# Performance work log

Measured on AMD Instinct MI355X. Metric: run time of the kernel, lower is better.

The kernel has to match this reference:

```python
import jax, jax.numpy as jnp
import numpy as np

NUM_HEADS = 16
HEAD_DIM = 64
MEMORY_SIZE = 65536
K_SIMILAR = 8
K_CONTIGUOUS = 2
SURPRISE_THRESHOLD = 0.5
EPS = 1e-8  # torch F.cosine_similarity eps


def setup_inputs() -> dict:
    key = jax.random.key(0)
    ks = jax.random.split(key, 6)
    B, H, S, HD = 4, NUM_HEADS, 8192, HEAD_DIM
    D = H * HD
    inputs = jax.random.normal(ks[0], (B, S, D), dtype=jnp.float32)
    q = jax.random.normal(ks[1], (B, H, S, HD), dtype=jnp.float32)
    k = jax.random.normal(ks[2], (B, H, S, HD), dtype=jnp.float32)
    v = jax.random.normal(ks[3], (B, H, S, HD), dtype=jnp.float32)
    attention_mask = jnp.ones((B, S), dtype=jnp.float32)
    events = jax.random.normal(ks[4], (MEMORY_SIZE, D), dtype=jnp.float32)
    return {"inputs": inputs, "q": q, "k": k, "v": v,
            "attention_mask": attention_mask, "events": events,
            "seq_len_q": 8192}


def _segment_mean(kf, seg, S):
    # kf: [S, D], seg: [S] int32 segment ids (exclusive cumsum of boundary mask)
    sums = jax.ops.segment_sum(kf, seg, num_segments=S)          # [S, D]
    cnts = jax.ops.segment_sum(jnp.ones_like(seg, jnp.float32), seg, num_segments=S)
    means = sums / jnp.maximum(cnts, 1.0)[:, None]
    return means, cnts


def reference(inputs, q, k, v, attention_mask, events, seq_len_q):
    B, H, S, HD = k.shape
    D = H * HD
    # flatten keys per token: [B, S, H*HD]
    kf = k.transpose(0, 2, 1, 3).reshape(B, S, D)

    # --- surprise scores: ||k_t - k_{t-1}|| padded with 0 at t=0 ---
    diffs = kf[:, 1:] - kf[:, :-1]
    norms = jnp.linalg.norm(diffs, axis=-1)                      # [B, S-1]
    surprise = jnp.pad(norms, ((0, 0), (1, 0)))                  # [B, S]

    # --- event segmentation (threshold = mean + c*std, unbiased std like torch) ---
    mean = jnp.mean(surprise, axis=1, keepdims=True)
    std = jnp.std(surprise, axis=1, ddof=1, keepdims=True)
    bmask = surprise > (mean + SURPRISE_THRESHOLD * std)
    bmask = bmask.at[:, -1].set(True)                            # last index is always a boundary
    bi = bmask.astype(jnp.int32)
    seg = jnp.cumsum(bi, axis=1) - bi                            # token t -> #boundaries before t

    # --- memory update: mean-pool keys within each event (scatter) ---
    new_events, event_lengths = jax.vmap(_segment_mean, in_axes=(0, 0, None))(kf, seg, S)
    # new_events: [B, S, D] (rows >= num_events are zero), event_lengths: [B, S]

    # --- retrieval: cosine sim of last-token key vs memory, top-k gather ---
    query = kf[:, -1]                                            # [B, D]
    qn = jnp.maximum(jnp.linalg.norm(query, axis=-1), EPS)       # [B]
    en = jnp.maximum(jnp.linalg.norm(events, axis=-1), EPS)      # [M]
    sims = (query @ events.T) / (qn[:, None] * en[None, :])      # [B, M]
    kt = min(K_SIMILAR + K_CONTIGUOUS, events.shape[0])
    _, idx = jax.lax.top_k(sims, kt)                             # [B, kt]

    ret = events[idx]                                            # [B, kt, D]
    ret = ret.reshape(B, kt, H, HD).transpose(0, 2, 1, 3)        # [B, H, kt, HD]
    ret_k, ret_v = ret, ret                                      # non-differential: v == k slice

    aug_k = jnp.concatenate([ret_k, k], axis=2)                  # [B, H, kt+S, HD]
    aug_v = jnp.concatenate([ret_v, v], axis=2)
    aug_mask = jnp.concatenate([jnp.ones((B, kt), attention_mask.dtype), attention_mask], axis=1)

    cp = seq_len_q - 1
    ret_pos = jnp.linspace(float(cp - kt), float(cp - 1), kt, dtype=jnp.float32)
    pos = jnp.arange(S, dtype=jnp.float32)
    aug_positions = jnp.broadcast_to(jnp.concatenate([ret_pos, pos]), (B, kt + S))

    return (inputs, q, aug_k, aug_v, aug_mask, aug_positions, new_events, event_lengths)
```

## Files before the change

kernel.cpp:

```cpp
#include <hip/hip_runtime.h>
#include <math.h>

#define BB 4
#define HH 16
#define SS 8192
#define HDD 64
#define DD 1024
#define MEM 65536
#define KT 10

static const long O0 = 0;
static const long O1 = 33554432;
static const long O2 = 67108864;
static const long O3 = 100704256;
static const long O4 = 134299648;
static const long O5 = 134332456;
static const long O6 = 134365264;
static const long O7 = 167919696;

#define WS_NEED_FUSED 5767168UL

typedef float __attribute__((ext_vector_type(4))) f4v;

static __device__ __forceinline__ void nt_store4(float4* p, float4 v) {
    f4v t; t.x = v.x; t.y = v.y; t.z = v.z; t.w = v.w;
    __builtin_nontemporal_store(t, (f4v*)p);
}
static __device__ __forceinline__ float4 nt_load4(const float4* p) {
    f4v t = __builtin_nontemporal_load((const f4v*)p);
    float4 v; v.x = t.x; v.y = t.y; v.z = t.z; v.w = t.w;
    return v;
}

#define N4REG 8388608L
__global__ __launch_bounds__(256) void bigmove_kernel(
        const float4* __restrict__ in0, const float4* __restrict__ q,
        const float4* __restrict__ k, const float4* __restrict__ v,
        float4* __restrict__ out4, double* __restrict__ partial,
        int do_part) {
    long i = (long)blockIdx.x * 256 + threadIdx.x;
    const long stride = (long)gridDim.x * 256;
    const long total = 4 * N4REG;
    for (; i < total; i += stride) {
        int region = (int)(i >> 23);
        long rel = i & (N4REG - 1);
        if (region == 0) {
            nt_store4(out4 + (O0 >> 2) + rel, nt_load4(in0 + rel));
        } else if (region == 1) {
            nt_store4(out4 + (O1 >> 2) + rel, nt_load4(q + rel));
        } else if (region == 3) {
            long chunk = rel >> 17;
            long r = rel & 131071;
            nt_store4(out4 + (O3 >> 2) + chunk * 131232 + 160 + r,
                      nt_load4(v + rel));
        } else {
            long chunk = rel >> 17;
            long r = rel & 131071;
            float4 cur = k[rel];
            nt_store4(out4 + (O2 >> 2) + chunk * 131232 + 160 + r, cur);
            if (do_part) {
                int s = (int)(r >> 4);
                if (s > 0) {
                    float4 pv = k[rel - 16];
                    double dx = (double)cur.x - (double)pv.x;
                    double dy = (double)cur.y - (double)pv.y;
                    double dz = (double)cur.z - (double)pv.z;
                    double dw = (double)cur.w - (double)pv.w;
                    double acc = dx * dx + dy * dy + dz * dz + dw * dw;
                    acc += __shfl_xor(acc, 1, 64);
                    acc += __shfl_xor(acc, 2, 64);
                    acc += __shfl_xor(acc, 4, 64);
                    acc += __shfl_xor(acc, 8, 64);
                    if ((threadIdx.x & 15) == 0)
                        partial[chunk * SS + s] = acc;
                }
            }
        }
    }
}

__global__ __launch_bounds__(256) void surprise_reduce_kernel(
        const double* __restrict__ partial, double* __restrict__ surprise) {
    int t = blockIdx.x * 256 + threadIdx.x;
    if (t >= BB * SS) return;
    int b = t >> 13;
    int s = t & (SS - 1);
    double acc = 0.0;
    if (s > 0) {
        for (int h = 0; h < HH; ++h)
            acc += partial[(((long)(b * HH + h)) << 13) + s];
    }
    surprise[t] = (s == 0) ? 0.0 : sqrt(acc);
}

__global__ __launch_bounds__(256) void surprise_fallback_kernel(
        const float* __restrict__ k, double* __restrict__ surprise) {
    int wid = (int)(((long)blockIdx.x * blockDim.x + threadIdx.x) >> 6);
    int lane = threadIdx.x & 63;
    if (wid >= BB * SS) return;
    int b = wid >> 13;
    int s = wid & (SS - 1);
    double acc = 0.0;
    if (s > 0) {
        const float* kb = k + (long)b * HH * SS * HDD;
        for (int h = 0; h < HH; ++h) {
            long off = ((long)h * SS + s) * HDD + lane;
            double d = (double)kb[off] - (double)kb[off - HDD];
            acc += d * d;
        }
        for (int m = 32; m >= 1; m >>= 1) acc += __shfl_xor(acc, m, 64);
    }
    if (lane == 0) surprise[wid] = (s == 0) ? 0.0 : sqrt(acc);
}

__global__ __launch_bounds__(1024) void stats_scan_kernel(
        const double* __restrict__ surprise, int* __restrict__ bpos,
        int* __restrict__ nseg) {
    int b = blockIdx.x;
    int tid = threadIdx.x;
    const double* sp = surprise + (long)b * SS;
    double loc[8];
    double sum = 0.0;
    for (int j = 0; j < 8; ++j) { loc[j] = sp[tid * 8 + j]; sum += loc[j]; }
    __shared__ double sd[1024];
    sd[tid] = sum;
    __syncthreads();
    for (int off = 512; off >= 1; off >>= 1) {
        if (tid < off) sd[tid] += sd[tid + off];
        __syncthreads();
    }
    double mean = sd[0] / SS;
    __syncthreads();
    double vs = 0.0;
    for (int j = 0; j < 8; ++j) { double d = loc[j] - mean; vs += d * d; }
    sd[tid] = vs;
    __syncthreads();
    for (int off = 512; off >= 1; off >>= 1) {
        if (tid < off) sd[tid] += sd[tid + off];
        __syncthreads();
    }
    double thr = mean + 0.5 * sqrt(sd[0] / (SS - 1));
    __syncthreads();

    int bi[8];
    int cnt = 0;
    for (int j = 0; j < 8; ++j) {
        int s = tid * 8 + j;
        bi[j] = (s == SS - 1) || (loc[j] > thr);
        cnt += bi[j];
    }
    __shared__ int si[1024];
    si[tid] = cnt;
    __syncthreads();
    for (int off = 1; off < 1024; off <<= 1) {
        int v = 0;
        if (tid >= off) v = si[tid - off];
        __syncthreads();
        si[tid] += v;
        __syncthreads();
    }
    int run = si[tid] - cnt;
    for (int j = 0; j < 8; ++j) {
        if (bi[j]) { bpos[(long)b * SS + run] = tid * 8 + j; ++run; }
    }
    if (tid == 1023) nseg[b] = si[1023];
}

__global__ __launch_bounds__(1024) void qnorm_kernel(
        const float* __restrict__ k, double* __restrict__ qn) {
    int b = blockIdx.x;
    int tid = threadIdx.x;
    float v = k[(((long)b * HH + (tid >> 6)) * SS + (SS - 1)) * HDD + (tid & 63)];
    __shared__ double sd[1024];
    sd[tid] = (double)v * (double)v;
    __syncthreads();
    for (int off = 512; off >= 1; off >>= 1) {
        if (tid < off) sd[tid] += sd[tid + off];
        __syncthreads();
    }
    if (tid == 0) qn[b] = fmax(sqrt(sd[0]), 1e-8);
}

__global__ __launch_bounds__(256) void sims_kernel(
        const float4* __restrict__ events4, const float* __restrict__ k,
        const double* __restrict__ qn, float* __restrict__ sims) {
    __shared__ float qls[4][BB][256];
    __shared__ double qns[BB];
    int tid = threadIdx.x;
    for (int j = tid; j < BB * DD; j += 256) {
        int b = j >> 10;
        int e = j & 1023;
        float val = k[(((long)b * HH + (e >> 6)) * SS + (SS - 1)) * HDD + (e & 63)];
        qls[e & 3][b][e >> 2] = val;
    }
    if (tid < BB) qns[tid] = qn[tid];
    __syncthreads();
    int w = tid >> 6;
    int lane = tid & 63;
    long e = (long)blockIdx.x * 4 + w;
    const float4* er = events4 + e * 256;
    double en = 0.0, d0 = 0.0, d1 = 0.0, d2 = 0.0, d3 = 0.0;
    for (int it = 0; it < 4; ++it) {
        int j4 = lane + it * 64;
        float4 ev = er[j4];
        double v0 = ev.x, v1 = ev.y, v2 = ev.z, v3 = ev.w;
        en += v0 * v0 + v1 * v1 + v2 * v2 + v3 * v3;
        d0 += v0 * (double)qls[0][0][j4] + v1 * (double)qls[1][0][j4] +
              v2 * (double)qls[2][0][j4] + v3 * (double)qls[3][0][j4];
        d1 += v0 * (double)qls[0][1][j4] + v1 * (double)qls[1][1][j4] +
              v2 * (double)qls[2][1][j4] + v3 * (double)qls[3][1][j4];
        d2 += v0 * (double)qls[0][2][j4] + v1 * (double)qls[1][2][j4] +
              v2 * (double)qls[2][2][j4] + v3 * (double)qls[3][2][j4];
        d3 += v0 * (double)qls[0][3][j4] + v1 * (double)qls[1][3][j4] +
              v2 * (double)qls[2][3][j4] + v3 * (double)qls[3][3][j4];
    }
    for (int m = 32; m >= 1; m >>= 1) {
        en += __shfl_xor(en, m, 64);
        d0 += __shfl_xor(d0, m, 64);
        d1 += __shfl_xor(d1, m, 64);
        d2 += __shfl_xor(d2, m, 64);
        d3 += __shfl_xor(d3, m, 64);
    }
    if (lane == 0) {
        double enn = fmax(sqrt(en), 1e-8);
        sims[0 * (long)MEM + e] = (float)(d0 / (qns[0] * enn));
        sims[1 * (long)MEM + e] = (float)(d1 / (qns[1] * enn));
        sims[2 * (long)MEM + e] = (float)(d2 / (qns[2] * enn));
        sims[3 * (long)MEM + e] = (float)(d3 / (qns[3] * enn));
    }
}

__global__ __launch_bounds__(256) void topk_part_kernel(
        const float* __restrict__ sims, float* __restrict__ cval,
        int* __restrict__ cidx) {
    int blk = blockIdx.x;
    int b = blk >> 4;
    int part = blk & 15;
    const float* sb = sims + (long)b * MEM + part * 4096;
    int base = part * 4096;
    int tid = threadIdx.x;
    __shared__ float bv[256];
    __shared__ int bix[256];
    __shared__ int chosen[KT];
    for (int p = 0; p < KT; ++p) {
        float best = -INFINITY;
        int bi = 0x7fffffff;
        for (int it = 0; it < 16; ++it) {
            int e = tid + it * 256;
            bool skip = false;
            for (int c = 0; c < p; ++c)
                if (chosen[c] == e) skip = true;
            if (skip) continue;
            float v = sb[e];
            if (v > best) { best = v; bi = e; }
        }
        bv[tid] = best;
        bix[tid] = bi;
        __syncthreads();
        for (int off = 128; off >= 1; off >>= 1) {
            if (tid < off) {
                if (bv[tid + off] > bv[tid] ||
                    (bv[tid + off] == bv[tid] && bix[tid + off] < bix[tid])) {
                    bv[tid] = bv[tid + off];
                    bix[tid] = bix[tid + off];
                }
            }
            __syncthreads();
        }
        if (tid == 0) {
            chosen[p] = bix[0];
            cval[blk * KT + p] = bv[0];
            cidx[blk * KT + p] = base + bix[0];
        }
        __syncthreads();
    }
}

__global__ __launch_bounds__(256) void topk_merge_kernel(
        const float* __restrict__ cval, const int* __restrict__ cidx,
        int* __restrict__ idxout) {
    int b = blockIdx.x;
    int tid = threadIdx.x;
    __shared__ float v[256];
    __shared__ int ix[256];
    float mv = -INFINITY;
    int mi = 0x7fffffff;
    if (tid < 160) { mv = cval[b * 160 + tid]; mi = cidx[b * 160 + tid]; }
    v[tid] = mv;
    ix[tid] = mi;
    __syncthreads();
    if (tid == 0) {
        for (int p = 0; p < KT; ++p) {
            float best = -INFINITY;
            int bi = 0x7fffffff;
            int bslot = 0;
            for (int j = 0; j < 160; ++j) {
                if (v[j] > best || (v[j] == best && ix[j] < bi)) {
                    best = v[j];
                    bi = ix[j];
                    bslot = j;
                }
            }
            idxout[b * KT + p] = bi;
            v[bslot] = -INFINITY;
            ix[bslot] = 0x7fffffff;
        }
    }
}

__global__ __launch_bounds__(1024) void gather_kernel(
        const float* __restrict__ events, const int* __restrict__ idxin,
        float* __restrict__ aug_k, float* __restrict__ aug_v) {
    int blk = blockIdx.x;
    int b = blk / KT;
    int t = blk % KT;
    int tid = threadIdx.x;
    int ev = idxin[b * KT + t];
    float v = events[(long)ev * DD + tid];
    int h = tid >> 6;
    int d = tid & 63;
    long dst = (((long)b * HH + h) * (SS + KT) + t) * HDD + d;
    aug_k[dst] = v;
    aug_v[dst] = v;
}

__global__ __launch_bounds__(256) void segmean_kernel(
        const float4* __restrict__ k4, const int* __restrict__ bpos,
        const int* __restrict__ nseg, float4* __restrict__ ne4,
        float* __restrict__ event_lengths) {
    int j = blockIdx.x;
    int b = blockIdx.y;
    int tid = threadIdx.x;
    float4* row = ne4 + ((long)b * SS + j) * 256;
    int ns = nseg[b];
    if (j >= ns) {
        nt_store4(row + tid, make_float4(0.f, 0.f, 0.f, 0.f));
        if (tid == 0) event_lengths[(long)b * SS + j] = 0.0f;
        return;
    }
    int start = (j == 0) ? 0 : bpos[(long)b * SS + j - 1] + 1;
    int end = bpos[(long)b * SS + j];
    const float4* kb = k4 + ((long)(b * HH + (tid >> 4)) * SS) * 16 + (tid & 15);
    double a0 = 0.0, a1 = 0.0, a2 = 0.0, a3 = 0.0;
    for (int s = start; s <= end; ++s) {
        float4 x = kb[(long)s * 16];
        a0 += (double)x.x;
        a1 += (double)x.y;
        a2 += (double)x.z;
        a3 += (double)x.w;
    }
    double inv = 1.0 / (double)(end - start + 1);
    nt_store4(row + tid, make_float4((float)(a0 * inv), (float)(a1 * inv),
                                     (float)(a2 * inv), (float)(a3 * inv)));
    if (tid == 0) event_lengths[(long)b * SS + j] = (float)(end - start + 1);
}

__global__ void maskpos_kernel(const float* __restrict__ amask,
                               const void* __restrict__ seqp,
                               float* __restrict__ out_mask,
                               float* __restrict__ out_pos) {
    int iv = ((const int*)seqp)[0];
    int seqlen;
    if (iv > 0 && iv < (1 << 24)) seqlen = iv;
    else seqlen = (int)(((const float*)seqp)[0]);
    int cp = seqlen - 1;
    int n = BB * (SS + KT);
    int i = blockIdx.x * blockDim.x + threadIdx.x;
    int stride = gridDim.x * blockDim.x;
    for (; i < n; i += stride) {
        int b = i / (SS + KT);
        int t = i - b * (SS + KT);
        out_mask[i] = (t < KT) ? 1.0f : amask[(long)b * SS + t - KT];
        out_pos[i] = (t < KT) ? (float)(cp - KT + t) : (float)(t - KT);
    }
}

extern "C" void kernel_launch(void* const* d_in, const int* in_sizes, int n_in,
                              void* d_out, int out_size, void* d_ws, size_t ws_size,
                              hipStream_t stream) {
    const float* in_inputs = (const float*)d_in[0];
    const float* in_q = (const float*)d_in[1];
    const float* in_k = (const float*)d_in[2];
    const float* in_v = (const float*)d_in[3];
    const float* in_amask = (const float*)d_in[4];
    const float* in_events = (const float*)d_in[5];
    const void* in_seq = d_in[6];
    float* out = (float*)d_out;

    char* ws = (char*)d_ws;
    double* surprise = (double*)ws;
    float* sims = (float*)(ws + 262144);
    int* bpos = (int*)(ws + 1310720);
    int* nseg = (int*)(ws + 1441792);
    int* idxw = (int*)(ws + 1441824);
    double* qn = (double*)(ws + 1442048);
    float* cval = (float*)(ws + 1442304);
    int* cidx = (int*)(ws + 1444864);
    double* partial = (double*)(ws + 1572864);

    const int fused = (ws_size >= WS_NEED_FUSED) ? 1 : 0;

    bigmove_kernel<<<4096, 256, 0, stream>>>(
        (const float4*)in_inputs, (const float4*)in_q, (const float4*)in_k,
        (const float4*)in_v, (float4*)out, partial, fused);
    if (fused) {
        surprise_reduce_kernel<<<BB * SS / 256, 256, 0, stream>>>(partial,
                                                                  surprise);
    } else {
        surprise_fallback_kernel<<<8192, 256, 0, stream>>>(in_k, surprise);
    }
    stats_scan_kernel<<<4, 1024, 0, stream>>>(surprise, bpos, nseg);
    qnorm_kernel<<<4, 1024, 0, stream>>>(in_k, qn);
    sims_kernel<<<MEM / 4, 256, 0, stream>>>((const float4*)in_events, in_k, qn,
                                             sims);
    topk_part_kernel<<<BB * 16, 256, 0, stream>>>(sims, cval, cidx);
    topk_merge_kernel<<<BB, 256, 0, stream>>>(cval, cidx, idxw);
    gather_kernel<<<BB * KT, 1024, 0, stream>>>(in_events, idxw, out + O2,
                                                out + O3);
    dim3 sg(SS, BB);
    segmean_kernel<<<sg, 256, 0, stream>>>((const float4*)in_k, bpos, nseg,
                                           (float4*)(out + O6), out + O7);
    maskpos_kernel<<<64, 256, 0, stream>>>(in_amask, in_seq, out + O4, out + O5);
}
```

Before: 525.6 us.

## Fuse copy, similarity and zero-fill into one kernel; fold surprise reduce into scan

Merges the bulk copy, cosine-similarity and zero-fill of the new-events output into one heterogeneous launch partitioned by block index. The surprise reduction now happens inside the stats/scan kernel, reading a transposed partial layout. Similarities switch from double to float and drop the query-norm division, since top-k ranking does not depend on it. Gather and mask/position kernels are merged, and segmean skips zero rows already written by the fused kernel. This cuts launches and lets similarity compute overlap with the bandwidth-bound copy, but changes sims values and may alter tie-breaking in top-k.

Result: faster. 501.9 us (-4.5%).

```diff
diff --git a/kernel.cpp b/kernel.cpp
--- a/kernel.cpp
+++ b/kernel.cpp
@@ -20,6 +20,8 @@
 
 #define WS_NEED_FUSED 5767168UL
 
+#define N4REG 8388608L
+
 typedef float __attribute__((ext_vector_type(4))) f4v;
 
 static __device__ __forceinline__ void nt_store4(float4* p, float4 v) {
@@ -32,65 +34,115 @@
     return v;
 }
 
-#define N4REG 8388608L
-__global__ __launch_bounds__(256) void bigmove_kernel(
+#define R0_BLOCKS 4096
+#define R1_BLOCKS 16384
+#define R2_BLOCKS 2048
+__global__ __launch_bounds__(256) void bigfused_kernel(
         const float4* __restrict__ in0, const float4* __restrict__ q,
-        const float4* __restrict__ k, const float4* __restrict__ v,
+        const float4* __restrict__ k4, const float* __restrict__ kf,
+        const float4* __restrict__ v, const float4* __restrict__ events4,
         float4* __restrict__ out4, double* __restrict__ partial,
-        int do_part) {
-    long i = (long)blockIdx.x * 256 + threadIdx.x;
-    const long stride = (long)gridDim.x * 256;
-    const long total = 4 * N4REG;
-    for (; i < total; i += stride) {
-        int region = (int)(i >> 23);
-        long rel = i & (N4REG - 1);
-        if (region == 0) {
-            nt_store4(out4 + (O0 >> 2) + rel, nt_load4(in0 + rel));
-        } else if (region == 1) {
-            nt_store4(out4 + (O1 >> 2) + rel, nt_load4(q + rel));
-        } else if (region == 3) {
-            long chunk = rel >> 17;
-            long r = rel & 131071;
-            nt_store4(out4 + (O3 >> 2) + chunk * 131232 + 160 + r,
-                      nt_load4(v + rel));
+        float* __restrict__ sims, int do_part) {
+    __shared__ float4 qls4[BB][256];
+    int blk = blockIdx.x;
+    int tid = threadIdx.x;
+    if (blk < R0_BLOCKS) {
+        int band = blk >> 10;
+        long i = ((long)(blk & 1023)) * 256 + tid;
+        const long bstride = 1024L * 256;
+        if (band == 0) {
+            for (; i < N4REG; i += bstride)
+                nt_store4(out4 + (O0 >> 2) + i, nt_load4(in0 + i));
+        } else if (band == 1) {
+            for (; i < N4REG; i += bstride)
+                nt_store4(out4 + (O1 >> 2) + i, nt_load4(q + i));
+        } else if (band == 3) {
+            for (; i < N4REG; i += bstride) {
+                long chunk = i >> 17;
+                long r = i & 131071;
+                nt_store4(out4 + (O3 >> 2) + chunk * 131232 + 160 + r,
+                          nt_load4(v + i));
+            }
         } else {
-            long chunk = rel >> 17;
-            long r = rel & 131071;
-            float4 cur = k[rel];
-            nt_store4(out4 + (O2 >> 2) + chunk * 131232 + 160 + r, cur);
-            if (do_part) {
-                int s = (int)(r >> 4);
-                if (s > 0) {
-                    float4 pv = k[rel - 16];
-                    double dx = (double)cur.x - (double)pv.x;
-                    double dy = (double)cur.y - (double)pv.y;
-                    double dz = (double)cur.z - (double)pv.z;
-                    double dw = (double)cur.w - (double)pv.w;
-                    double acc = dx * dx + dy * dy + dz * dz + dw * dw;
-                    acc += __shfl_xor(acc, 1, 64);
-                    acc += __shfl_xor(acc, 2, 64);
-                    acc += __shfl_xor(acc, 4, 64);
-                    acc += __shfl_xor(acc, 8, 64);
-                    if ((threadIdx.x & 15) == 0)
-                        partial[chunk * SS + s] = acc;
+            for (; i < N4REG; i += bstride) {
+                long chunk = i >> 17;
+                long r = i & 131071;
+                float4 cur = k4[i];
+                nt_store4(out4 + (O2 >> 2) + chunk * 131232 + 160 + r, cur);
+                if (do_part) {
+                    int s = (int)(r >> 4);
+                    if (s > 0) {
+                        float4 pv = k4[i - 16];
+                        double dx = (double)cur.x - (double)pv.x;
+                        double dy = (double)cur.y - (double)pv.y;
+                        double dz = (double)cur.z - (double)pv.z;
+                        double dw = (double)cur.w - (double)pv.w;
+                        double acc = dx * dx + dy * dy + dz * dz + dw * dw;
+                        acc += __shfl_xor(acc, 1, 64);
+                        acc += __shfl_xor(acc, 2, 64);
+                        acc += __shfl_xor(acc, 4, 64);
+                        acc += __shfl_xor(acc, 8, 64);
+                        if ((tid & 15) == 0) {
+                            int b = (int)(chunk >> 4);
+                            int h = (int)(chunk & 15);
+                            partial[((long)b * SS + s) * HH + h] = acc;
+                        }
+                    }
                 }
             }
         }
-    }
-}
-
-__global__ __launch_bounds__(256) void surprise_reduce_kernel(
-        const double* __restrict__ partial, double* __restrict__ surprise) {
-    int t = blockIdx.x * 256 + threadIdx.x;
-    if (t >= BB * SS) return;
-    int b = t >> 13;
-    int s = t & (SS - 1);
-    double acc = 0.0;
-    if (s > 0) {
-        for (int h = 0; h < HH; ++h)
-            acc += partial[(((long)(b * HH + h)) << 13) + s];
-    }
-    surprise[t] = (s == 0) ? 0.0 : sqrt(acc);
+    } else if (blk < R0_BLOCKS + R1_BLOCKS) {
+        for (int j = tid; j < BB * 256; j += 256) {
+            int b = j >> 8;
+            int f4i = j & 255;
+            qls4[b][f4i] =
+                k4[((long)(b * HH + (f4i >> 4)) * SS + (SS - 1)) * 16 + (f4i & 15)];
+        }
+        __syncthreads();
+        int w = tid >> 6;
+        int lane = tid & 63;
+        long e = (long)(blk - R0_BLOCKS) * 4 + w;
+        const float4* er = events4 + e * 256;
+        float en = 0.f, d0 = 0.f, d1 = 0.f, d2 = 0.f, d3 = 0.f;
+#pragma unroll
+        for (int it = 0; it < 4; ++it) {
+            int j4 = lane + it * 64;
+            float4 ev = nt_load4(er + j4);
+            en += ev.x * ev.x + ev.y * ev.y + ev.z * ev.z + ev.w * ev.w;
+            float4 q0 = qls4[0][j4];
+            d0 += ev.x * q0.x + ev.y * q0.y + ev.z * q0.z + ev.w * q0.w;
+            float4 q1 = qls4[1][j4];
+            d1 += ev.x * q1.x + ev.y * q1.y + ev.z * q1.z + ev.w * q1.w;
+            float4 q2 = qls4[2][j4];
+            d2 += ev.x * q2.x + ev.y * q2.y + ev.z * q2.z + ev.w * q2.w;
+            float4 q3 = qls4[3][j4];
+            d3 += ev.x * q3.x + ev.y * q3.y + ev.z * q3.z + ev.w * q3.w;
+        }
+        for (int m = 32; m >= 1; m >>= 1) {
+            en += __shfl_xor(en, m, 64);
+            d0 += __shfl_xor(d0, m, 64);
+            d1 += __shfl_xor(d1, m, 64);
+            d2 += __shfl_xor(d2, m, 64);
+            d3 += __shfl_xor(d3, m, 64);
+        }
+        if (lane == 0) {
+            float enn = fmaxf(sqrtf(en), 1e-8f);
+            sims[0 * (long)MEM + e] = d0 / enn;
+            sims[1 * (long)MEM + e] = d1 / enn;
+            sims[2 * (long)MEM + e] = d2 / enn;
+            sims[3 * (long)MEM + e] = d3 / enn;
+        }
+    } else {
+        long i = ((long)(blk - R0_BLOCKS - R1_BLOCKS)) * 256 + tid;
+        const long stride = (long)R2_BLOCKS * 256;
+        const float4 z = make_float4(0.f, 0.f, 0.f, 0.f);
+        for (; i < 8396800L; i += stride) {
+            if (i < 8388608L)
+                nt_store4(out4 + (O6 >> 2) + i, z);
+            else
+                nt_store4(out4 + (O7 >> 2) + (i - 8388608L), z);
+        }
+    }
 }
 
 __global__ __launch_bounds__(256) void surprise_fallback_kernel(
@@ -114,14 +166,28 @@
 }
 
 __global__ __launch_bounds__(1024) void stats_scan_kernel(
-        const double* __restrict__ surprise, int* __restrict__ bpos,
-        int* __restrict__ nseg) {
+        const double* __restrict__ partial, const double* __restrict__ surprise,
+        int* __restrict__ bpos, int* __restrict__ nseg, int fused) {
     int b = blockIdx.x;
     int tid = threadIdx.x;
-    const double* sp = surprise + (long)b * SS;
     double loc[8];
     double sum = 0.0;
-    for (int j = 0; j < 8; ++j) { loc[j] = sp[tid * 8 + j]; sum += loc[j]; }
+    if (fused) {
+        const double* pb = partial + (long)b * SS * HH;
+        for (int j = 0; j < 8; ++j) {
+            int s = tid * 8 + j;
+            double acc = 0.0;
+            if (s > 0) {
+                const double* row = pb + (long)s * HH;
+                for (int h = 0; h < HH; ++h) acc += row[h];
+            }
+            loc[j] = (s == 0) ? 0.0 : sqrt(acc);
+            sum += loc[j];
+        }
+    } else {
+        const double* sp = surprise + (long)b * SS;
+        for (int j = 0; j < 8; ++j) { loc[j] = sp[tid * 8 + j]; sum += loc[j]; }
+    }
     __shared__ double sd[1024];
     sd[tid] = sum;
     __syncthreads();
@@ -164,70 +230,6 @@
         if (bi[j]) { bpos[(long)b * SS + run] = tid * 8 + j; ++run; }
     }
     if (tid == 1023) nseg[b] = si[1023];
-}
-
-__global__ __launch_bounds__(1024) void qnorm_kernel(
-        const float* __restrict__ k, double* __restrict__ qn) {
-    int b = blockIdx.x;
-    int tid = threadIdx.x;
-    float v = k[(((long)b * HH + (tid >> 6)) * SS + (SS - 1)) * HDD + (tid & 63)];
-    __shared__ double sd[1024];
-    sd[tid] = (double)v * (double)v;
-    __syncthreads();
-    for (int off = 512; off >= 1; off >>= 1) {
-        if (tid < off) sd[tid] += sd[tid + off];
-        __syncthreads();
-    }
-    if (tid == 0) qn[b] = fmax(sqrt(sd[0]), 1e-8);
-}
-
-__global__ __launch_bounds__(256) void sims_kernel(
-        const float4* __restrict__ events4, const float* __restrict__ k,
-        const double* __restrict__ qn, float* __restrict__ sims) {
-    __shared__ float qls[4][BB][256];
-    __shared__ double qns[BB];
-    int tid = threadIdx.x;
-    for (int j = tid; j < BB * DD; j += 256) {
-        int b = j >> 10;
-        int e = j & 1023;
-        float val = k[(((long)b * HH + (e >> 6)) * SS + (SS - 1)) * HDD + (e & 63)];
-        qls[e & 3][b][e >> 2] = val;
-    }
-    if (tid < BB) qns[tid] = qn[tid];
-    __syncthreads();
-    int w = tid >> 6;
-    int lane = tid & 63;
-    long e = (long)blockIdx.x * 4 + w;
-    const float4* er = events4 + e * 256;
-    double en = 0.0, d0 = 0.0, d1 = 0.0, d2 = 0.0, d3 = 0.0;
-    for (int it = 0; it < 4; ++it) {
-        int j4 = lane + it * 64;
-        float4 ev = er[j4];
-        double v0 = ev.x, v1 = ev.y, v2 = ev.z, v3 = ev.w;
-        en += v0 * v0 + v1 * v1 + v2 * v2 + v3 * v3;
-        d0 += v0 * (double)qls[0][0][j4] + v1 * (double)qls[1][0][j4] +
-              v2 * (double)qls[2][0][j4] + v3 * (double)qls[3][0][j4];
-        d1 += v0 * (double)qls[0][1][j4] + v1 * (double)qls[1][1][j4] +
-              v2 * (double)qls[2][1][j4] + v3 * (double)qls[3][1][j4];
-        d2 += v0 * (double)qls[0][2][j4] + v1 * (double)qls[1][2][j4] +
-              v2 * (double)qls[2][2][j4] + v3 * (double)qls[3][2][j4];
-        d3 += v0 * (double)qls[0][3][j4] + v1 * (double)qls[1][3][j4] +
-              v2 * (double)qls[2][3][j4] + v3 * (double)qls[3][3][j4];
-    }
-    for (int m = 32; m >= 1; m >>= 1) {
-        en += __shfl_xor(en, m, 64);
-        d0 += __shfl_xor(d0, m, 64);
-        d1 += __shfl_xor(d1, m, 64);
-        d2 += __shfl_xor(d2, m, 64);
-        d3 += __shfl_xor(d3, m, 64);
-    }
-    if (lane == 0) {
-        double enn = fmax(sqrt(en), 1e-8);
-        sims[0 * (long)MEM + e] = (float)(d0 / (qns[0] * enn));
-        sims[1 * (long)MEM + e] = (float)(d1 / (qns[1] * enn));
-        sims[2 * (long)MEM + e] = (float)(d2 / (qns[2] * enn));
-        sims[3 * (long)MEM + e] = (float)(d3 / (qns[3] * enn));
-    }
 }
 
 __global__ __launch_bounds__(256) void topk_part_kernel(
@@ -308,20 +310,41 @@
     }
 }
 
-__global__ __launch_bounds__(1024) void gather_kernel(
+__global__ __launch_bounds__(256) void tail_kernel(
         const float* __restrict__ events, const int* __restrict__ idxin,
-        float* __restrict__ aug_k, float* __restrict__ aug_v) {
+        const float* __restrict__ amask, const void* __restrict__ seqp,
+        float* __restrict__ out) {
     int blk = blockIdx.x;
-    int b = blk / KT;
-    int t = blk % KT;
-    int tid = threadIdx.x;
-    int ev = idxin[b * KT + t];
-    float v = events[(long)ev * DD + tid];
-    int h = tid >> 6;
-    int d = tid & 63;
-    long dst = (((long)b * HH + h) * (SS + KT) + t) * HDD + d;
-    aug_k[dst] = v;
-    aug_v[dst] = v;
+    int tid = threadIdx.x;
+    if (blk < BB * KT) {
+        int b = blk / KT;
+        int t = blk % KT;
+        int ev = idxin[b * KT + t];
+        for (int c = 0; c < 4; ++c) {
+            int j = tid + c * 256;
+            float vv = events[(long)ev * DD + j];
+            int h = j >> 6;
+            int d = j & 63;
+            long dst = (((long)b * HH + h) * (SS + KT) + t) * HDD + d;
+            out[O2 + dst] = vv;
+            out[O3 + dst] = vv;
+        }
+    } else {
+        int iv = ((const int*)seqp)[0];
+        int seqlen;
+        if (iv > 0 && iv < (1 << 24)) seqlen = iv;
+        else seqlen = (int)(((const float*)seqp)[0]);
+        int cp = seqlen - 1;
+        int n = BB * (SS + KT);
+        int i = (blk - BB * KT) * 256 + tid;
+        int stride = 64 * 256;
+        for (; i < n; i += stride) {
+            int b = i / (SS + KT);
+            int t = i - b * (SS + KT);
+            out[O4 + i] = (t < KT) ? 1.0f : amask[(long)b * SS + t - KT];
+            out[O5 + i] = (t < KT) ? (float)(cp - KT + t) : (float)(t - KT);
+        }
+    }
 }
 
 __global__ __launch_bounds__(256) void segmean_kernel(
@@ -330,14 +353,10 @@
         float* __restrict__ event_lengths) {
     int j = blockIdx.x;
     int b = blockIdx.y;
+    int ns = nseg[b];
+    if (j >= ns) return;
     int tid = threadIdx.x;
     float4* row = ne4 + ((long)b * SS + j) * 256;
-    int ns = nseg[b];
-    if (j >= ns) {
-        nt_store4(row + tid, make_float4(0.f, 0.f, 0.f, 0.f));
-        if (tid == 0) event_lengths[(long)b * SS + j] = 0.0f;
-        return;
-    }
     int start = (j == 0) ? 0 : bpos[(long)b * SS + j - 1] + 1;
     int end = bpos[(long)b * SS + j];
     const float4* kb = k4 + ((long)(b * HH + (tid >> 4)) * SS) * 16 + (tid & 15);
@@ -353,26 +372,6 @@
     nt_store4(row + tid, make_float4((float)(a0 * inv), (float)(a1 * inv),
                                      (float)(a2 * inv), (float)(a3 * inv)));
     if (tid == 0) event_lengths[(long)b * SS + j] = (float)(end - start + 1);
-}
-
-__global__ void maskpos_kernel(const float* __restrict__ amask,
-                               const void* __restrict__ seqp,
-                               float* __restrict__ out_mask,
-                               float* __restrict__ out_pos) {
-    int iv = ((const int*)seqp)[0];
-    int seqlen;
-    if (iv > 0 && iv < (1 << 24)) seqlen = iv;
-    else seqlen = (int)(((const float*)seqp)[0]);
-    int cp = seqlen - 1;
-    int n = BB * (SS + KT);
-    int i = blockIdx.x * blockDim.x + threadIdx.x;
-    int stride = gridDim.x * blockDim.x;
-    for (; i < n; i += stride) {
-        int b = i / (SS + KT);
-        int t = i - b * (SS + KT);
-        out_mask[i] = (t < KT) ? 1.0f : amask[(long)b * SS + t - KT];
-        out_pos[i] = (t < KT) ? (float)(cp - KT + t) : (float)(t - KT);
-    }
 }
 
 extern "C" void kernel_launch(void* const* d_in, const int* in_sizes, int n_in,
@@ -393,32 +392,25 @@
     int* bpos = (int*)(ws + 1310720);
     int* nseg = (int*)(ws + 1441792);
     int* idxw = (int*)(ws + 1441824);
-    double* qn = (double*)(ws + 1442048);
     float* cval = (float*)(ws + 1442304);
     int* cidx = (int*)(ws + 1444864);
     double* partial = (double*)(ws + 1572864);
 
     const int fused = (ws_size >= WS_NEED_FUSED) ? 1 : 0;
 
-    bigmove_kernel<<<4096, 256, 0, stream>>>(
+    bigfused_kernel<<<R0_BLOCKS + R1_BLOCKS + R2_BLOCKS, 256, 0, stream>>>(
         (const float4*)in_inputs, (const float4*)in_q, (const float4*)in_k,
-        (const float4*)in_v, (float4*)out, partial, fused);
-    if (fused) {
-        surprise_reduce_kernel<<<BB * SS / 256, 256, 0, stream>>>(partial,
-                                                                  surprise);
-    } else {
+        in_k, (const float4*)in_v, (const float4*)in_events, (float4*)out,
+        partial, sims, fused);
+    if (!fused)
         surprise_fallback_kernel<<<8192, 256, 0, stream>>>(in_k, surprise);
-    }
-    stats_scan_kernel<<<4, 1024, 0, stream>>>(surprise, bpos, nseg);
-    qnorm_kernel<<<4, 1024, 0, stream>>>(in_k, qn);
-    sims_kernel<<<MEM / 4, 256, 0, stream>>>((const float4*)in_events, in_k, qn,
-                                             sims);
+    stats_scan_kernel<<<4, 1024, 0, stream>>>(partial, surprise, bpos, nseg,
+                                              fused);
     topk_part_kernel<<<BB * 16, 256, 0, stream>>>(sims, cval, cidx);
     topk_merge_kernel<<<BB, 256, 0, stream>>>(cval, cidx, idxw);
-    gather_kernel<<<BB * KT, 1024, 0, stream>>>(in_events, idxw, out + O2,
-                                                out + O3);
+    tail_kernel<<<BB * KT + 64, 256, 0, stream>>>(in_events, idxw, in_amask,
+                                                  in_seq, out);
     dim3 sg(SS, BB);
     segmean_kernel<<<sg, 256, 0, stream>>>((const float4*)in_k, bpos, nseg,
                                            (float4*)(out + O6), out + O7);
-    maskpos_kernel<<<64, 256, 0, stream>>>(in_amask, in_seq, out + O4, out + O5);
-}
+}
```
